# Kernel optimization log

Hardware: AMD Instinct MI355X
Metric: run time of the kernel (lower is better)

The kernel has to match this reference:

```python
import jax, jax.numpy as jnp
import numpy as np
from jax import lax

MEANING_SZ = 512
ARTIC = 64
EMBED = 256
H1 = 512
H2 = 512
SLEN = 32


def _lstm(xs, h0, c0, Wih, Whh, bih, bhh):
    """Single-layer LSTM, torch gate order (i, f, g, o). xs: [S, B, I]."""
    def step(carry, x):
        h, c = carry
        gates = x @ Wih.T + h @ Whh.T + bih + bhh  # [B, 4H]
        i, f, g, o = jnp.split(gates, 4, axis=-1)
        c = jax.nn.sigmoid(f) * c + jax.nn.sigmoid(i) * jnp.tanh(g)
        h = jax.nn.sigmoid(o) * jnp.tanh(c)
        return (h, c), h
    (h, c), ys = lax.scan(step, (h0, c0), xs)
    return ys, (h, c)


def setup_inputs() -> dict:
    key = jax.random.key(0)
    ks = jax.random.split(key, 16)
    s = 0.05
    inp = {
        "ms": jnp.arange(MEANING_SZ, dtype=jnp.int64 if jax.config.jax_enable_x64 else jnp.int32),
        "batches": 16,
        "embedding": jax.random.normal(ks[0], (MEANING_SZ, EMBED), jnp.float32) * s,
        "enc_Wih": jax.random.normal(ks[1], (4 * H1, EMBED), jnp.float32) * s,
        "enc_Whh": jax.random.normal(ks[2], (4 * H1, H1), jnp.float32) * s,
        "enc_bih": jnp.zeros((4 * H1,), jnp.float32),
        "enc_bhh": jnp.zeros((4 * H1,), jnp.float32),
        "enc_init": jax.random.normal(ks[3], (2, H1), jnp.float32) * s,
        "dec_Wih": jax.random.normal(ks[4], (4 * H2, ARTIC), jnp.float32) * s,
        "dec_Whh": jax.random.normal(ks[5], (4 * H2, H2), jnp.float32) * s,
        "dec_bih": jnp.zeros((4 * H2,), jnp.float32),
        "dec_bhh": jnp.zeros((4 * H2,), jnp.float32),
        "dec_init": jax.random.normal(ks[6], (2, H2), jnp.float32) * s,
        "W_param": jax.random.normal(ks[7], (H1, 2 * ARTIC), jnp.float32) * s,
        "W_out": jax.random.normal(ks[8], (H2, MEANING_SZ), jnp.float32) * s,
    }
    return inp


def reference(ms, batches, embedding, enc_Wih, enc_Whh, enc_bih, enc_bhh, enc_init,
              dec_Wih, dec_Whh, dec_bih, dec_bhh, dec_init, W_param, W_out):
    M = embedding.shape[0]
    # --- encoder ---
    embed = embedding[ms]                                   # [M, E]
    xs = jnp.broadcast_to(embed, (SLEN,) + embed.shape)     # same embed repeated S times
    h0 = jnp.broadcast_to(enc_init[0], (M, H1))
    c0 = jnp.broadcast_to(enc_init[1], (M, H1))
    ys, _ = _lstm(xs, h0, c0, enc_Wih, enc_Whh, enc_bih, enc_bhh)  # [S, M, H1]
    params = jax.nn.softplus(jnp.einsum('smh,hp->smp', ys, W_param))  # [S, M, 2A]
    alpha = params[..., 0::2]                               # [S, M, A]
    beta = params[..., 1::2]                                # [S, M, A]
    # --- vectorized Beta reparameterized sampling (replaces triple python loop) ---
    key = jax.random.key(42)
    samp = jax.random.beta(key, alpha, beta, shape=(batches,) + alpha.shape)  # [B, S, M, A]
    # torch.cat along dim=-2 with batch-major blocks -> [S, B*M, A]
    signals = samp.transpose(1, 0, 2, 3).reshape(SLEN, batches * M, ARTIC)
    # --- decoder ---
    hB = jnp.broadcast_to(dec_init[0], (batches * M, H2))
    cB = jnp.broadcast_to(dec_init[1], (batches * M, H2))
    _, (h_last, _) = _lstm(signals, hB, cB, dec_Wih, dec_Whh, dec_bih, dec_bhh)
    logits = h_last @ W_out                                 # [B*M, M]
    return jax.nn.softmax(logits, axis=-1)
```

## Files before the change

### kernel.cpp

```cpp
#include <hip/hip_runtime.h>
#include <cstdint>
#include <cstddef>


namespace {

constexpr int MZ = 512;
constexpr int EMB = 256;
constexpr int H = 512;
constexpr int SL = 32;
constexpr int BT = 16;
constexpr int AR = 64;
constexpr int GG = 4 * H;
constexpr int RD = BT * MZ;
constexpr int SAMP_BLOCKS = 128;
constexpr int MFMA_BLOCKS = (H / 32) * (RD / 128);
constexpr int LROW = 40;

typedef float f32x4 __attribute__((ext_vector_type(4)));
typedef __bf16 bf16x8 __attribute__((ext_vector_type(8)));

struct KK { unsigned a, b; };

__host__ __device__ constexpr unsigned rotl32(unsigned v, int r) {
  return (v << r) | (v >> (32 - r));
}

__host__ __device__ constexpr KK tf(unsigned k0, unsigned k1, unsigned x0, unsigned x1) {
  unsigned k2 = k0 ^ k1 ^ 0x1BD11BDAu;
  x0 += k0; x1 += k1;
  x0 += x1; x1 = rotl32(x1,13); x1 ^= x0;
  x0 += x1; x1 = rotl32(x1,15); x1 ^= x0;
  x0 += x1; x1 = rotl32(x1,26); x1 ^= x0;
  x0 += x1; x1 = rotl32(x1, 6); x1 ^= x0;
  x0 += k1; x1 += k2 + 1u;
  x0 += x1; x1 = rotl32(x1,17); x1 ^= x0;
  x0 += x1; x1 = rotl32(x1,29); x1 ^= x0;
  x0 += x1; x1 = rotl32(x1,16); x1 ^= x0;
  x0 += x1; x1 = rotl32(x1,24); x1 ^= x0;
  x0 += k2; x1 += k0 + 2u;
  x0 += x1; x1 = rotl32(x1,13); x1 ^= x0;
  x0 += x1; x1 = rotl32(x1,15); x1 ^= x0;
  x0 += x1; x1 = rotl32(x1,26); x1 ^= x0;
  x0 += x1; x1 = rotl32(x1, 6); x1 ^= x0;
  x0 += k0; x1 += k1 + 3u;
  x0 += x1; x1 = rotl32(x1,17); x1 ^= x0;
  x0 += x1; x1 = rotl32(x1,29); x1 ^= x0;
  x0 += x1; x1 = rotl32(x1,16); x1 ^= x0;
  x0 += x1; x1 = rotl32(x1,24); x1 ^= x0;
  x0 += k1; x1 += k2 + 4u;
  x0 += x1; x1 = rotl32(x1,13); x1 ^= x0;
  x0 += x1; x1 = rotl32(x1,15); x1 ^= x0;
  x0 += x1; x1 = rotl32(x1,26); x1 ^= x0;
  x0 += x1; x1 = rotl32(x1, 6); x1 ^= x0;
  x0 += k2; x1 += k0 + 5u;
  return KK{x0, x1};
}

constexpr KK KEYA = tf(0u, 42u, 0u, 0u);
constexpr KK KEYB = tf(0u, 42u, 0u, 1u);

__device__ __forceinline__ void split2(KK k, KK& o0, KK& o1) {
  o0 = tf(k.a, k.b, 0u, 0u); o1 = tf(k.a, k.b, 0u, 1u);
}

__device__ __forceinline__ void split3(KK k, KK& o0, KK& o1, KK& o2) {
  o0 = tf(k.a, k.b, 0u, 0u); o1 = tf(k.a, k.b, 0u, 1u); o2 = tf(k.a, k.b, 0u, 2u);
}

__device__ __forceinline__ KK elem_key(KK gk, unsigned j) {
  return tf(gk.a, gk.b, 0u, j);
}

__device__ __forceinline__ unsigned rb32(KK k) {
  KK r = tf(k.a, k.b, 0u, 0u);
  return r.a ^ r.b;
}

__device__ __forceinline__ float u01_from_bits(unsigned bits) {
  return __uint_as_float(0x3F800000u | (bits >> 9)) - 1.0f;
}
__device__ __forceinline__ float uniform01(KK k) {
  return u01_from_bits(rb32(k));
}

__device__ float erfinv_xla(float x) {
  float xx = __fmul_rn(x, x);
  float w = -log1pf(-xx);
  float p;
  if (w < 5.0f) {
    w = __fsub_rn(w, 2.5f);
    p = 2.81022636e-08f;
    p = __fadd_rn(3.43273939e-07f, __fmul_rn(p, w));
    p = __fadd_rn(-3.5233877e-06f, __fmul_rn(p, w));
    p = __fadd_rn(-4.39150654e-06f, __fmul_rn(p, w));
    p = __fadd_rn(0.00021858087f, __fmul_rn(p, w));
    p = __fadd_rn(-0.00125372503f, __fmul_rn(p, w));
    p = __fadd_rn(-0.00417768164f, __fmul_rn(p, w));
    p = __fadd_rn(0.246640727f, __fmul_rn(p, w));
    p = __fadd_rn(1.50140941f, __fmul_rn(p, w));
  } else {
    w = __fsub_rn(__fsqrt_rn(w), 3.0f);
    p = -0.000200214257f;
    p = __fadd_rn(0.000100950558f, __fmul_rn(p, w));
    p = __fadd_rn(0.00134934322f, __fmul_rn(p, w));
    p = __fadd_rn(-0.00367342844f, __fmul_rn(p, w));
    p = __fadd_rn(0.00573950773f, __fmul_rn(p, w));
    p = __fadd_rn(-0.0076224613f, __fmul_rn(p, w));
    p = __fadd_rn(0.00943887047f, __fmul_rn(p, w));
    p = __fadd_rn(1.00167406f, __fmul_rn(p, w));
    p = __fadd_rn(2.83297682f, __fmul_rn(p, w));
  }
  return __fmul_rn(p, x);
}

__device__ __forceinline__ float normal_f(KK k) {
  float f = u01_from_bits(rb32(k));
  const float lo = __uint_as_float(0xBF7FFFFFu);
  float u = __fadd_rn(__fmul_rn(f, 2.0f), lo);
  u = fmaxf(lo, u);
  return __fmul_rn(__uint_as_float(0x3FB504F3u), erfinv_xla(u));
}

__device__ float loggamma_one(KK ekey, float alpha_orig) {
  KK key, sub;
  split2(ekey, key, sub);
  float u_boost = uniform01(sub);
  const bool boost = (alpha_orig >= 1.0f);
  const float al = boost ? alpha_orig : __fadd_rn(alpha_orig, 1.0f);
  const float third = (float)(1.0 / 3.0);
  const float d = __fsub_rn(al, third);
  const float c = __fdiv_rn(third, __fsqrt_rn(d));
  float X, V;
  for (;;) {
    KK nk, xk, uk;
    split3(key, nk, xk, uk);
    key = nk;
    float x, v;
    KK kk = xk;
    do {
      KK k2, ns;
      split2(kk, k2, ns);
      kk = k2;
      x = normal_f(ns);
      v = __fadd_rn(1.0f, __fmul_rn(x, c));
    } while (v <= 0.0f);
    X = __fmul_rn(x, x);
    V = __fmul_rn(__fmul_rn(v, v), v);
    float U = uniform01(uk);
    float sq = __fsub_rn(1.0f, __fmul_rn(0.0331f, __fmul_rn(X, X)));
    if (U < sq) break;
    float rhs = __fadd_rn(__fmul_rn(0.5f, X),
                          __fmul_rn(d, __fadd_rn(__fsub_rn(1.0f, V), logf(V))));
    if (logf(U) < rhs) break;
  }
  float ls = __fadd_rn(logf(d), logf(V));
  if (!boost)
    ls = __fadd_rn(ls, __fdiv_rn(log1pf(-u_boost), alpha_orig));
  return ls;
}

__device__ __forceinline__ float sigm(float x) { return 1.0f / (1.0f + expf(-x)); }

__device__ __forceinline__ unsigned short f2bf(float x) {
  unsigned u = __float_as_uint(x);
  unsigned r = (u + 0x7fffu + ((u >> 16) & 1u)) >> 16;
  return (unsigned short)r;
}
__device__ __forceinline__ float bf2f(unsigned short h) {
  return __uint_as_float(((unsigned)h) << 16);
}
__device__ __forceinline__ void split_bf(float x, unsigned short& hi, unsigned short& lo) {
  hi = f2bf(x);
  lo = f2bf(x - bf2f(hi));
}

__device__ __forceinline__ void beta_sample(const float* __restrict__ alphaA,
                                            const float* __restrict__ betaA,
                                            unsigned short* __restrict__ sigHi,
                                            unsigned short* __restrict__ sigLo,
                                            unsigned idx, int s) {
  unsigned r = idx >> 6;
  unsigned j = idx & 63u;
  unsigned b = r >> 9;
  unsigned m = r & 511u;
  size_t ab = ((size_t)s * MZ + m) * AR + j;
  float alpha = alphaA[ab];
  float beta = betaA[ab];
  unsigned jl = ((b * 32u + (unsigned)s) * 512u + m) * 64u + j;
  float lga = loggamma_one(elem_key(KEYA, jl), alpha);
  float lgb = loggamma_one(elem_key(KEYB, jl), beta);
  float lm = fmaxf(lga, lgb);
  float ea = expf(__fsub_rn(lga, lm));
  float eb = expf(__fsub_rn(lgb, lm));
  float sv = __fdiv_rn(ea, __fadd_rn(ea, eb));
  split_bf(sv, sigHi[idx], sigLo[idx]);
}

}


__global__ __launch_bounds__(256) void fill_sentinel_r17(float* o, int n) {
  int i = blockIdx.x * 256 + threadIdx.x;
  if (i < n) o[i] = 12345.0f;
}

__global__ __launch_bounds__(256) void init_states_r17(const float* __restrict__ encI,
                                                       const float* __restrict__ decI,
                                                       float* __restrict__ hE, float* __restrict__ cE,
                                                       float* __restrict__ hD, float* __restrict__ cD) {
  int idx = blockIdx.x * 256 + threadIdx.x;
  int u = idx & (H - 1);
  if (idx < MZ * H) { hE[idx] = encI[u]; cE[idx] = encI[H + u]; }
  hD[idx] = decI[u]; cD[idx] = decI[H + u];
}

__global__ __launch_bounds__(256) void prep_dec_r17(const float* __restrict__ Wih,
                                                    const float* __restrict__ Whh,
                                                    const float* __restrict__ b1,
                                                    const float* __restrict__ b2,
                                                    unsigned short* __restrict__ WihHi,
                                                    unsigned short* __restrict__ WihLo,
                                                    unsigned short* __restrict__ WhhHi,
                                                    unsigned short* __restrict__ WhhLo,
                                                    float* __restrict__ bsum,
                                                    const float* __restrict__ hD,
                                                    unsigned short* __restrict__ hHi,
                                                    unsigned short* __restrict__ hLo) {
  int idx = blockIdx.x * 256 + threadIdx.x;
  split_bf(Whh[idx], WhhHi[idx], WhhLo[idx]);
  if (idx < GG * AR) split_bf(Wih[idx], WihHi[idx], WihLo[idx]);
  if (idx < GG) bsum[idx] = b1[idx] + b2[idx];
  for (int i = idx; i < RD * H; i += GG * H) split_bf(hD[i], hHi[i], hLo[i]);
}

template <int MODE>
__global__ __launch_bounds__(256) void gemm_abt_r17(const float* __restrict__ A,
                                                    const float* __restrict__ B,
                                                    float* __restrict__ C,
                                                    const float* __restrict__ X1,
                                                    const float* __restrict__ X2,
                                                    int M, int N, int K) {
  __shared__ float As[16][68];
  __shared__ float Bs[16][68];
  int tid = threadIdx.x;
  int tx = tid & 15, ty = tid >> 4;
  int n0 = blockIdx.x * 64, m0 = blockIdx.y * 64;
  int lr = tid >> 2, lk4 = (tid & 3) * 4;
  float acc[4][4] = {};
  for (int k0 = 0; k0 < K; k0 += 16) {
    float4 a4 = *reinterpret_cast<const float4*>(A + (size_t)(m0 + lr) * K + k0 + lk4);
    float4 b4 = *reinterpret_cast<const float4*>(B + (size_t)(n0 + lr) * K + k0 + lk4);
    __syncthreads();
    As[lk4 + 0][lr] = a4.x; As[lk4 + 1][lr] = a4.y; As[lk4 + 2][lr] = a4.z; As[lk4 + 3][lr] = a4.w;
    Bs[lk4 + 0][lr] = b4.x; Bs[lk4 + 1][lr] = b4.y; Bs[lk4 + 2][lr] = b4.z; Bs[lk4 + 3][lr] = b4.w;
    __syncthreads();
#pragma unroll
    for (int k = 0; k < 16; ++k) {
      float av[4], bv[4];
#pragma unroll
      for (int i = 0; i < 4; ++i) av[i] = As[k][ty * 4 + i];
#pragma unroll
      for (int j = 0; j < 4; ++j) bv[j] = Bs[k][tx * 4 + j];
#pragma unroll
      for (int i = 0; i < 4; ++i)
#pragma unroll
        for (int j = 0; j < 4; ++j) acc[i][j] = fmaf(av[i], bv[j], acc[i][j]);
    }
  }
#pragma unroll
  for (int i = 0; i < 4; ++i) {
    int m = m0 + ty * 4 + i;
#pragma unroll
    for (int j = 0; j < 4; ++j) {
      int n = n0 + tx * 4 + j;
      float v = acc[i][j];
      if (MODE == 1) v += X1[n] + X2[n];
      if (MODE == 2) v += X1[(size_t)m * N + n];
      C[(size_t)m * N + n] = v;
    }
  }
}

__global__ __launch_bounds__(256) void mfma_step_r17(
    const unsigned short* __restrict__ sigHi, const unsigned short* __restrict__ sigLo,
    const unsigned short* __restrict__ hHiIn, const unsigned short* __restrict__ hLoIn,
    const unsigned short* __restrict__ WihHi, const unsigned short* __restrict__ WihLo,
    const unsigned short* __restrict__ WhhHi, const unsigned short* __restrict__ WhhLo,
    const float* __restrict__ bsum,
    float* __restrict__ hD, float* __restrict__ cD,
    unsigned short* __restrict__ hHiOut, unsigned short* __restrict__ hLoOut,
    int writeHF,
    const float* __restrict__ alphaA, const float* __restrict__ betaA,
    unsigned short* __restrict__ sigHiNext, unsigned short* __restrict__ sigLoNext,
    int sNext, int nSamp) {
  __shared__ __align__(16) unsigned short AhiS[128 * LROW];
  __shared__ __align__(16) unsigned short AloS[128 * LROW];
  __shared__ __align__(16) unsigned short BhiS[128 * LROW];
  __shared__ __align__(16) unsigned short BloS[128 * LROW];
  int bid = blockIdx.x;
  if (bid < nSamp) {
    unsigned base = bid * 256 + threadIdx.x;
    unsigned stride = (unsigned)nSamp * 256;
    for (unsigned idx = base; idx < (unsigned)(RD * AR); idx += stride)
      beta_sample(alphaA, betaA, sigHiNext, sigLoNext, idx, sNext);
    return;
  }
  bid -= nSamp;
  int ub = bid & 15;
  int mb = bid >> 4;
  int mbBase = mb * 128;
  int ubBase = ub * 32;
  int tid = threadIdx.x;
  int lane = tid & 63, wid = tid >> 6;
  int wr = wid >> 1, wu = wid & 1;
  int lr = lane & 15;
  int lk = (lane >> 4) * 8;
  int srow = tid >> 2;
  int scol = (tid & 3) * 8;
  f32x4 acc[4][4] = {};
  for (int ks = 0; ks < 18; ++ks) {
    int k0 = ks * 32;
    const unsigned short* Ah; const unsigned short* Al;
    const unsigned short* Bh; const unsigned short* Bl;
    int K, kk;
    if (k0 < 64) { Ah = sigHi; Al = sigLo; Bh = WihHi; Bl = WihLo; K = AR; kk = k0; }
    else         { Ah = hHiIn; Al = hLoIn; Bh = WhhHi; Bl = WhhLo; K = H;  kk = k0 - 64; }
    __syncthreads();
#pragma unroll
    for (int q = 0; q < 2; ++q) {
      int row = q * 64 + srow;
      size_t asrc = (size_t)(mbBase + row) * K + kk + scol;
      int g = row >> 5, uu = row & 31;
      size_t bsrc = (size_t)(g * 512 + ubBase + uu) * K + kk + scol;
      int ldst = row * LROW + scol;
      *reinterpret_cast<bf16x8*>(&AhiS[ldst]) = *reinterpret_cast<const bf16x8*>(Ah + asrc);
      *reinterpret_cast<bf16x8*>(&AloS[ldst]) = *reinterpret_cast<const bf16x8*>(Al + asrc);
      *reinterpret_cast<bf16x8*>(&BhiS[ldst]) = *reinterpret_cast<const bf16x8*>(Bh + bsrc);
      *reinterpret_cast<bf16x8*>(&BloS[ldst]) = *reinterpret_cast<const bf16x8*>(Bl + bsrc);
    }
    __syncthreads();
    bf16x8 ah[4], al[4], bh[4], bl[4];
#pragma unroll
    for (int f = 0; f < 4; ++f) {
      int arow = wr * 64 + f * 16 + lr;
      ah[f] = *reinterpret_cast<const bf16x8*>(&AhiS[arow * LROW + lk]);
      al[f] = *reinterpret_cast<const bf16x8*>(&AloS[arow * LROW + lk]);
      int brow = f * 32 + wu * 16 + lr;
      bh[f] = *reinterpret_cast<const bf16x8*>(&BhiS[brow * LROW + lk]);
      bl[f] = *reinterpret_cast<const bf16x8*>(&BloS[brow * LROW + lk]);
    }
#pragma unroll
    for (int i = 0; i < 4; ++i)
#pragma unroll
      for (int g = 0; g < 4; ++g) {
        acc[i][g] = __builtin_amdgcn_mfma_f32_16x16x32_bf16(ah[i], bh[g], acc[i][g], 0, 0, 0);
        acc[i][g] = __builtin_amdgcn_mfma_f32_16x16x32_bf16(ah[i], bl[g], acc[i][g], 0, 0, 0);
        acc[i][g] = __builtin_amdgcn_mfma_f32_16x16x32_bf16(al[i], bh[g], acc[i][g], 0, 0, 0);
      }
  }
  int m0 = mbBase + wr * 64;
  int crow = (lane >> 4) * 4;
  int u = ubBase + wu * 16 + (lane & 15);
  float bi = bsum[u], bff = bsum[u + 512], bg = bsum[u + 1024], bo = bsum[u + 1536];
#pragma unroll
  for (int i = 0; i < 4; ++i) {
#pragma unroll
    for (int r = 0; r < 4; ++r) {
      int m = m0 + i * 16 + crow + r;
      size_t idx = (size_t)m * H + u;
      float gi = acc[i][0][r] + bi;
      float gf = acc[i][1][r] + bff;
      float gg = acc[i][2][r] + bg;
      float go = acc[i][3][r] + bo;
      float cn = sigm(gf) * cD[idx] + sigm(gi) * tanhf(gg);
      float hn = sigm(go) * tanhf(cn);
      cD[idx] = cn;
      if (writeHF) hD[idx] = hn;
      split_bf(hn, hHiOut[idx], hLoOut[idx]);
    }
  }
}

template <int EPI>
__global__ __launch_bounds__(256) void gemm_ab_r17(const float* __restrict__ A,
                                                   const float* __restrict__ B,
                                                   float* __restrict__ C0,
                                                   float* __restrict__ C1,
                                                   int M, int N, int K) {
  __shared__ float As[16][68];
  __shared__ float Bs[16][68];
  int tid = threadIdx.x;
  int tx = tid & 15, ty = tid >> 4;
  int n0 = blockIdx.x * 64, m0 = blockIdx.y * 64;
  int lr = tid >> 2, lk4 = (tid & 3) * 4;
  int bk = tid >> 4, bn4 = (tid & 15) * 4;
  float acc[4][4] = {};
  for (int k0 = 0; k0 < K; k0 += 16) {
    float4 a4 = *reinterpret_cast<const float4*>(A + (size_t)(m0 + lr) * K + k0 + lk4);
    float4 b4 = *reinterpret_cast<const float4*>(B + (size_t)(k0 + bk) * N + n0 + bn4);
    __syncthreads();
    As[lk4 + 0][lr] = a4.x; As[lk4 + 1][lr] = a4.y; As[lk4 + 2][lr] = a4.z; As[lk4 + 3][lr] = a4.w;
    *reinterpret_cast<float4*>(&Bs[bk][bn4]) = b4;
    __syncthreads();
#pragma unroll
    for (int k = 0; k < 16; ++k) {
      float av[4], bv[4];
#pragma unroll
      for (int i = 0; i < 4; ++i) av[i] = As[k][ty * 4 + i];
#pragma unroll
      for (int j = 0; j < 4; ++j) bv[j] = Bs[k][tx * 4 + j];
#pragma unroll
      for (int i = 0; i < 4; ++i)
#pragma unroll
        for (int j = 0; j < 4; ++j) acc[i][j] = fmaf(av[i], bv[j], acc[i][j]);
    }
  }
#pragma unroll
  for (int i = 0; i < 4; ++i) {
    size_t m = (size_t)(m0 + ty * 4 + i);
#pragma unroll
    for (int j = 0; j < 4; ++j) {
      int n = n0 + tx * 4 + j;
      float v = acc[i][j];
      if (EPI == 0) {
        C0[m * N + n] = v;
      } else {
        float sp = fmaxf(v, 0.0f) + log1pf(expf(-fabsf(v)));
        if (n & 1) C1[m * (N / 2) + (n >> 1)] = sp;
        else       C0[m * (N / 2) + (n >> 1)] = sp;
      }
    }
  }
}

__global__ __launch_bounds__(256) void lstm_update_r17(float* __restrict__ h, float* __restrict__ c,
                                                       const float* __restrict__ gates,
                                                       float* __restrict__ ysOut) {
  int idx = blockIdx.x * 256 + threadIdx.x;
  int r = idx >> 9, u = idx & (H - 1);
  const float* g = gates + (size_t)r * GG;
  float gi = g[u], gf = g[u + H], gg = g[u + 2 * H], go = g[u + 3 * H];
  float cn = sigm(gf) * c[idx] + sigm(gi) * tanhf(gg);
  float hn = sigm(go) * tanhf(cn);
  c[idx] = cn; h[idx] = hn;
  if (ysOut) ysOut[idx] = hn;
}

__global__ __launch_bounds__(256) void sample_beta_r17(const float* __restrict__ alphaA,
                                                       const float* __restrict__ betaA,
                                                       unsigned short* __restrict__ sigHi,
                                                       unsigned short* __restrict__ sigLo,
                                                       int s) {
  unsigned idx = blockIdx.x * 256 + threadIdx.x;
  beta_sample(alphaA, betaA, sigHi, sigLo, idx, s);
}

__global__ __launch_bounds__(256) void softmax_rows_r17(const float* __restrict__ L,
                                                        float* __restrict__ O) {
  __shared__ float red[8];
  int r = blockIdx.x;
  const float* row = L + (size_t)r * H;
  int t = threadIdx.x;
  float a = row[t], b = row[t + 256];
  float m = fmaxf(a, b);
#pragma unroll
  for (int o = 1; o < 64; o <<= 1) m = fmaxf(m, __shfl_xor(m, o));
  if ((t & 63) == 0) red[t >> 6] = m;
  __syncthreads();
  m = fmaxf(fmaxf(red[0], red[1]), fmaxf(red[2], red[3]));
  float e0 = expf(a - m), e1 = expf(b - m);
  float s = e0 + e1;
#pragma unroll
  for (int o = 1; o < 64; o <<= 1) s += __shfl_xor(s, o);
  if ((t & 63) == 0) red[4 + (t >> 6)] = s;
  __syncthreads();
  s = red[4] + red[5] + red[6] + red[7];
  O[(size_t)r * H + t] = e0 / s;
  O[(size_t)r * H + t + 256] = e1 / s;
}


extern "C" void kernel_launch(void* const* d_in, const int* in_sizes, int n_in,
                              void* d_out, int out_size, void* d_ws, size_t ws_size,
                              hipStream_t stream) {
  (void)in_sizes; (void)n_in;
  const float* embedding = (const float*)d_in[2];
  const float* eWih = (const float*)d_in[3];
  const float* eWhh = (const float*)d_in[4];
  const float* ebih = (const float*)d_in[5];
  const float* ebhh = (const float*)d_in[6];
  const float* eInit = (const float*)d_in[7];
  const float* dWih = (const float*)d_in[8];
  const float* dWhh = (const float*)d_in[9];
  const float* dbih = (const float*)d_in[10];
  const float* dbhh = (const float*)d_in[11];
  const float* dInit = (const float*)d_in[12];
  const float* Wp = (const float*)d_in[13];
  const float* Wo = (const float*)d_in[14];
  float* out = (float*)d_out;
  float* w = (float*)d_ws;

  size_t o = 0;
  float* xW     = w + o; o += (size_t)MZ * GG;
  float* hE     = w + o; o += (size_t)MZ * H;
  float* cE     = w + o; o += (size_t)MZ * H;
  float* ys     = w + o; o += (size_t)SL * MZ * H;
  float* alphaA = w + o; o += (size_t)SL * MZ * AR;
  float* betaA  = w + o; o += (size_t)SL * MZ * AR;
  float* hD     = w + o; o += (size_t)RD * H;
  float* cD     = w + o; o += (size_t)RD * H;
  float* regB   = w + o; o += (size_t)RD * GG / 4;
  float* logits = w + o; o += (size_t)RD * H;
  float* sig1F  = w + o; o += (size_t)RD * AR;
  if (ws_size < o * sizeof(float)) {
    fill_sentinel_r17<<<(out_size + 255) / 256, 256, 0, stream>>>(out, out_size);
    return;
  }

  unsigned short* sig0Hi = (unsigned short*)ys;
  unsigned short* sig0Lo = sig0Hi + (size_t)RD * AR;
  unsigned short* h0Hi  = sig0Lo + (size_t)RD * AR;
  unsigned short* h0Lo  = h0Hi + (size_t)RD * H;
  unsigned short* WihHi = h0Lo + (size_t)RD * H;
  unsigned short* WihLo = WihHi + (size_t)GG * AR;
  unsigned short* WhhHi = WihLo + (size_t)GG * AR;
  unsigned short* WhhLo = WhhHi + (size_t)GG * H;
  float* bsum = (float*)(WhhLo + (size_t)GG * H);
  unsigned short* h1Hi = (unsigned short*)regB;
  unsigned short* h1Lo = h1Hi + (size_t)RD * H;
  unsigned short* sig1Hi = (unsigned short*)sig1F;
  unsigned short* sig1Lo = sig1Hi + (size_t)RD * AR;

  init_states_r17<<<(RD * H) / 256, 256, 0, stream>>>(eInit, dInit, hE, cE, hD, cD);

  float* egates = logits;
  gemm_abt_r17<1><<<dim3(GG / 64, MZ / 64), 256, 0, stream>>>(embedding, eWih, xW, ebih, ebhh, MZ, GG, EMB);
  for (int s = 0; s < SL; ++s) {
    gemm_abt_r17<2><<<dim3(GG / 64, MZ / 64), 256, 0, stream>>>(hE, eWhh, egates, xW, nullptr, MZ, GG, H);
    lstm_update_r17<<<(MZ * H) / 256, 256, 0, stream>>>(hE, cE, egates, ys + (size_t)s * MZ * H);
  }

  gemm_ab_r17<1><<<dim3(128 / 64, (SL * MZ) / 64), 256, 0, stream>>>(ys, Wp, alphaA, betaA, SL * MZ, 128, H);

  prep_dec_r17<<<(GG * H) / 256, 256, 0, stream>>>(dWih, dWhh, dbih, dbhh,
                                                   WihHi, WihLo, WhhHi, WhhLo, bsum,
                                                   hD, h0Hi, h0Lo);

  sample_beta_r17<<<(RD * AR) / 256, 256, 0, stream>>>(alphaA, betaA, sig0Hi, sig0Lo, 0);

  for (int s = 0; s < SL; ++s) {
    const unsigned short* sHi = (s & 1) ? sig1Hi : sig0Hi;
    const unsigned short* sLo = (s & 1) ? sig1Lo : sig0Lo;
    unsigned short* snHi = (s & 1) ? sig0Hi : sig1Hi;
    unsigned short* snLo = (s & 1) ? sig0Lo : sig1Lo;
    const unsigned short* hiIn = (s & 1) ? h1Hi : h0Hi;
    const unsigned short* loIn = (s & 1) ? h1Lo : h0Lo;
    unsigned short* hiOut = (s & 1) ? h0Hi : h1Hi;
    unsigned short* loOut = (s & 1) ? h0Lo : h1Lo;
    int nSamp = (s < SL - 1) ? SAMP_BLOCKS : 0;
    mfma_step_r17<<<nSamp + MFMA_BLOCKS, 256, 0, stream>>>(
        sHi, sLo, hiIn, loIn, WihHi, WihLo, WhhHi, WhhLo, bsum,
        hD, cD, hiOut, loOut, (s == SL - 1) ? 1 : 0,
        alphaA, betaA, snHi, snLo, s + 1, nSamp);
  }

  gemm_ab_r17<0><<<dim3(H / 64, RD / 64), 256, 0, stream>>>(hD, Wo, logits, nullptr, RD, H, H);
  softmax_rows_r17<<<RD, 256, 0, stream>>>(logits, out);
}
```

Measured before the change: 5.080 ms.

## Run decoder LSTM as persistent cooperative kernel with grid sync and register cell state

Replaces the 32 per-step decoder kernel launches with one cooperative persistent kernel of 1024 blocks that loops over time steps and separates them with grid.sync. The cell state now stays in registers instead of going to global memory, and every block samples its share of the next step's Beta noise. Block-to-tile mapping is arranged by XCD, and the LDS row pitch shrinks from 40 to 36. The risks are grid-sync cost, occupancy limits for cooperative launch (it falls back to the old path on failure), and possible LDS bank conflicts with the new pitch.

```diff
diff --git a/kernel.cpp b/kernel.cpp
--- a/kernel.cpp
+++ b/kernel.cpp
@@ -1,7 +1,10 @@
 #include <hip/hip_runtime.h>
+#include <hip/hip_cooperative_groups.h>
 #include <cstdint>
 #include <cstddef>
 
+
+namespace cg = cooperative_groups;
 
 namespace {
 
@@ -13,9 +16,9 @@
 constexpr int AR = 64;
 constexpr int GG = 4 * H;
 constexpr int RD = BT * MZ;
+constexpr int LROW = 36;
 constexpr int SAMP_BLOCKS = 128;
 constexpr int MFMA_BLOCKS = (H / 32) * (RD / 128);
-constexpr int LROW = 40;
 
 typedef float f32x4 __attribute__((ext_vector_type(4)));
 typedef __bf16 bf16x8 __attribute__((ext_vector_type(8)));
@@ -197,15 +200,19 @@
   split_bf(sv, sigHi[idx], sigLo[idx]);
 }
 
-}
-
-
-__global__ __launch_bounds__(256) void fill_sentinel_r17(float* o, int n) {
+struct StepPtrs {
+  const unsigned short *sHi, *sLo, *hInHi, *hInLo;
+};
+
+}
+
+
+__global__ __launch_bounds__(256) void fill_sentinel_r19(float* o, int n) {
   int i = blockIdx.x * 256 + threadIdx.x;
   if (i < n) o[i] = 12345.0f;
 }
 
-__global__ __launch_bounds__(256) void init_states_r17(const float* __restrict__ encI,
+__global__ __launch_bounds__(256) void init_states_r19(const float* __restrict__ encI,
                                                        const float* __restrict__ decI,
                                                        float* __restrict__ hE, float* __restrict__ cE,
                                                        float* __restrict__ hD, float* __restrict__ cD) {
@@ -215,7 +222,7 @@
   hD[idx] = decI[u]; cD[idx] = decI[H + u];
 }
 
-__global__ __launch_bounds__(256) void prep_dec_r17(const float* __restrict__ Wih,
+__global__ __launch_bounds__(256) void prep_dec_r19(const float* __restrict__ Wih,
                                                     const float* __restrict__ Whh,
                                                     const float* __restrict__ b1,
                                                     const float* __restrict__ b2,
@@ -235,7 +242,7 @@
 }
 
 template <int MODE>
-__global__ __launch_bounds__(256) void gemm_abt_r17(const float* __restrict__ A,
+__global__ __launch_bounds__(256) void gemm_abt_r19(const float* __restrict__ A,
                                                     const float* __restrict__ B,
                                                     float* __restrict__ C,
                                                     const float* __restrict__ X1,
@@ -282,7 +289,125 @@
   }
 }
 
-__global__ __launch_bounds__(256) void mfma_step_r17(
+__global__ __launch_bounds__(256, 4) void dec_persist_r19(
+    unsigned short* sig0Hi, unsigned short* sig0Lo,
+    unsigned short* sig1Hi, unsigned short* sig1Lo,
+    unsigned short* h0Hi, unsigned short* h0Lo,
+    unsigned short* h1Hi, unsigned short* h1Lo,
+    const unsigned short* __restrict__ WihHi, const unsigned short* __restrict__ WihLo,
+    const unsigned short* __restrict__ WhhHi, const unsigned short* __restrict__ WhhLo,
+    const float* __restrict__ bsum, float* __restrict__ hD,
+    const float* __restrict__ cInit,
+    const float* __restrict__ alphaA, const float* __restrict__ betaA) {
+  __shared__ __align__(16) unsigned short AhiS[128 * LROW];
+  __shared__ __align__(16) unsigned short AloS[128 * LROW];
+  __shared__ __align__(16) unsigned short BhiS[128 * LROW];
+  __shared__ __align__(16) unsigned short BloS[128 * LROW];
+  cg::grid_group grid = cg::this_grid();
+  int bid = blockIdx.x;
+  int xcd = bid & 7, idxx = bid >> 3;
+  int mb = xcd * 8 + (idxx >> 4);
+  int ub = idxx & 15;
+  int mbBase = mb * 128;
+  int ubBase = ub * 32;
+  int tid = threadIdx.x;
+  int lane = tid & 63, wid = tid >> 6;
+  int wr = wid >> 1, wu = wid & 1;
+  int lr = lane & 15;
+  int lk = (lane >> 4) * 8;
+  int srow = tid >> 2;
+  int scol = (tid & 3) * 8;
+  int m0 = mbBase + wr * 64;
+  int crow = (lane >> 4) * 4;
+  int u = ubBase + wu * 16 + (lane & 15);
+  float bi = bsum[u], bff = bsum[u + 512], bg = bsum[u + 1024], bo = bsum[u + 1536];
+  float creg[4][4];
+  {
+    float c0 = cInit[u];
+#pragma unroll
+    for (int i = 0; i < 4; ++i)
+#pragma unroll
+      for (int r = 0; r < 4; ++r) creg[i][r] = c0;
+  }
+  for (int s = 0; s < SL; ++s) {
+    const unsigned short *sHi, *sLo, *hInHi, *hInLo;
+    unsigned short *hOutHi, *hOutLo, *snHi, *snLo;
+    if (s & 1) {
+      sHi = sig1Hi; sLo = sig1Lo; hInHi = h1Hi; hInLo = h1Lo;
+      hOutHi = h0Hi; hOutLo = h0Lo; snHi = sig0Hi; snLo = sig0Lo;
+    } else {
+      sHi = sig0Hi; sLo = sig0Lo; hInHi = h0Hi; hInLo = h0Lo;
+      hOutHi = h1Hi; hOutLo = h1Lo; snHi = sig1Hi; snLo = sig1Lo;
+    }
+    if (s < SL - 1) {
+      unsigned base = (unsigned)bid * 256 + tid;
+      beta_sample(alphaA, betaA, snHi, snLo, base, s + 1);
+      beta_sample(alphaA, betaA, snHi, snLo, base + 262144u, s + 1);
+    }
+    f32x4 acc[4][4] = {};
+    for (int ks = 0; ks < 18; ++ks) {
+      int k0 = ks * 32;
+      const unsigned short* Ah; const unsigned short* Al;
+      const unsigned short* Bh; const unsigned short* Bl;
+      int K, kk;
+      if (k0 < 64) { Ah = sHi; Al = sLo; Bh = WihHi; Bl = WihLo; K = AR; kk = k0; }
+      else         { Ah = hInHi; Al = hInLo; Bh = WhhHi; Bl = WhhLo; K = H; kk = k0 - 64; }
+      __syncthreads();
+#pragma unroll
+      for (int q = 0; q < 2; ++q) {
+        int row = q * 64 + srow;
+        size_t asrc = (size_t)(mbBase + row) * K + kk + scol;
+        int g = row >> 5, uu = row & 31;
+        size_t bsrc = (size_t)(g * 512 + ubBase + uu) * K + kk + scol;
+        int ldst = row * LROW + scol;
+        *reinterpret_cast<bf16x8*>(&AhiS[ldst]) = *reinterpret_cast<const bf16x8*>(Ah + asrc);
+        *reinterpret_cast<bf16x8*>(&AloS[ldst]) = *reinterpret_cast<const bf16x8*>(Al + asrc);
+        *reinterpret_cast<bf16x8*>(&BhiS[ldst]) = *reinterpret_cast<const bf16x8*>(Bh + bsrc);
+        *reinterpret_cast<bf16x8*>(&BloS[ldst]) = *reinterpret_cast<const bf16x8*>(Bl + bsrc);
+      }
+      __syncthreads();
+      bf16x8 ah[4], al[4], bh[4], bl[4];
+#pragma unroll
+      for (int f = 0; f < 4; ++f) {
+        int arow = wr * 64 + f * 16 + lr;
+        ah[f] = *reinterpret_cast<const bf16x8*>(&AhiS[arow * LROW + lk]);
+        al[f] = *reinterpret_cast<const bf16x8*>(&AloS[arow * LROW + lk]);
+        int brow = f * 32 + wu * 16 + lr;
+        bh[f] = *reinterpret_cast<const bf16x8*>(&BhiS[brow * LROW + lk]);
+        bl[f] = *reinterpret_cast<const bf16x8*>(&BloS[brow * LROW + lk]);
+      }
+#pragma unroll
+      for (int i = 0; i < 4; ++i)
+#pragma unroll
+        for (int g = 0; g < 4; ++g) {
+          acc[i][g] = __builtin_amdgcn_mfma_f32_16x16x32_bf16(ah[i], bh[g], acc[i][g], 0, 0, 0);
+          acc[i][g] = __builtin_amdgcn_mfma_f32_16x16x32_bf16(ah[i], bl[g], acc[i][g], 0, 0, 0);
+          acc[i][g] = __builtin_amdgcn_mfma_f32_16x16x32_bf16(al[i], bh[g], acc[i][g], 0, 0, 0);
+        }
+    }
+#pragma unroll
+    for (int i = 0; i < 4; ++i) {
+#pragma unroll
+      for (int r = 0; r < 4; ++r) {
+        int m = m0 + i * 16 + crow + r;
+        size_t idx = (size_t)m * H + u;
+        float gi = acc[i][0][r] + bi;
+        float gf = acc[i][1][r] + bff;
+        float gg = acc[i][2][r] + bg;
+        float go = acc[i][3][r] + bo;
+        float cn = sigm(gf) * creg[i][r] + sigm(gi) * tanhf(gg);
+        float hn = sigm(go) * tanhf(cn);
+        creg[i][r] = cn;
+        if (s == SL - 1) hD[idx] = hn;
+        split_bf(hn, hOutHi[idx], hOutLo[idx]);
+      }
+    }
+    __threadfence();
+    grid.sync();
+  }
+}
+
+__global__ __launch_bounds__(256) void mfma_step_r19(
     const unsigned short* __restrict__ sigHi, const unsigned short* __restrict__ sigLo,
     const unsigned short* __restrict__ hHiIn, const unsigned short* __restrict__ hLoIn,
     const unsigned short* __restrict__ WihHi, const unsigned short* __restrict__ WihLo,
@@ -383,7 +508,7 @@
 }
 
 template <int EPI>
-__global__ __launch_bounds__(256) void gemm_ab_r17(const float* __restrict__ A,
+__global__ __launch_bounds__(256) void gemm_ab_r19(const float* __restrict__ A,
                                                    const float* __restrict__ B,
                                                    float* __restrict__ C0,
                                                    float* __restrict__ C1,
@@ -434,7 +559,7 @@
   }
 }
 
-__global__ __launch_bounds__(256) void lstm_update_r17(float* __restrict__ h, float* __restrict__ c,
+__global__ __launch_bounds__(256) void lstm_update_r19(float* __restrict__ h, float* __restrict__ c,
                                                        const float* __restrict__ gates,
                                                        float* __restrict__ ysOut) {
   int idx = blockIdx.x * 256 + threadIdx.x;
@@ -447,7 +572,7 @@
   if (ysOut) ysOut[idx] = hn;
 }
 
-__global__ __launch_bounds__(256) void sample_beta_r17(const float* __restrict__ alphaA,
+__global__ __launch_bounds__(256) void sample_beta_r19(const float* __restrict__ alphaA,
                                                        const float* __restrict__ betaA,
                                                        unsigned short* __restrict__ sigHi,
                                                        unsigned short* __restrict__ sigLo,
@@ -456,7 +581,7 @@
   beta_sample(alphaA, betaA, sigHi, sigLo, idx, s);
 }
 
-__global__ __launch_bounds__(256) void softmax_rows_r17(const float* __restrict__ L,
+__global__ __launch_bounds__(256) void softmax_rows_r19(const float* __restrict__ L,
                                                         float* __restrict__ O) {
   __shared__ float red[8];
   int r = blockIdx.x;
@@ -514,7 +639,7 @@
   float* logits = w + o; o += (size_t)RD * H;
   float* sig1F  = w + o; o += (size_t)RD * AR;
   if (ws_size < o * sizeof(float)) {
-    fill_sentinel_r17<<<(out_size + 255) / 256, 256, 0, stream>>>(out, out_size);
+    fill_sentinel_r19<<<(out_size + 255) / 256, 256, 0, stream>>>(out, out_size);
     return;
   }
 
@@ -532,39 +657,51 @@
   unsigned short* sig1Hi = (unsigned short*)sig1F;
   unsigned short* sig1Lo = sig1Hi + (size_t)RD * AR;
 
-  init_states_r17<<<(RD * H) / 256, 256, 0, stream>>>(eInit, dInit, hE, cE, hD, cD);
+  init_states_r19<<<(RD * H) / 256, 256, 0, stream>>>(eInit, dInit, hE, cE, hD, cD);
 
   float* egates = logits;
-  gemm_abt_r17<1><<<dim3(GG / 64, MZ / 64), 256, 0, stream>>>(embedding, eWih, xW, ebih, ebhh, MZ, GG, EMB);
+  gemm_abt_r19<1><<<dim3(GG / 64, MZ / 64), 256, 0, stream>>>(embedding, eWih, xW, ebih, ebhh, MZ, GG, EMB);
   for (int s = 0; s < SL; ++s) {
-    gemm_abt_r17<2><<<dim3(GG / 64, MZ / 64), 256, 0, stream>>>(hE, eWhh, egates, xW, nullptr, MZ, GG, H);
-    lstm_update_r17<<<(MZ * H) / 256, 256, 0, stream>>>(hE, cE, egates, ys + (size_t)s * MZ * H);
-  }
-
-  gemm_ab_r17<1><<<dim3(128 / 64, (SL * MZ) / 64), 256, 0, stream>>>(ys, Wp, alphaA, betaA, SL * MZ, 128, H);
-
-  prep_dec_r17<<<(GG * H) / 256, 256, 0, stream>>>(dWih, dWhh, dbih, dbhh,
+    gemm_abt_r19<2><<<dim3(GG / 64, MZ / 64), 256, 0, stream>>>(hE, eWhh, egates, xW, nullptr, MZ, GG, H);
+    lstm_update_r19<<<(MZ * H) / 256, 256, 0, stream>>>(hE, cE, egates, ys + (size_t)s * MZ * H);
+  }
+
+  gemm_ab_r19<1><<<dim3(128 / 64, (SL * MZ) / 64), 256, 0, stream>>>(ys, Wp, alphaA, betaA, SL * MZ, 128, H);
+
+  prep_dec_r19<<<(GG * H) / 256, 256, 0, stream>>>(dWih, dWhh, dbih, dbhh,
                                                    WihHi, WihLo, WhhHi, WhhLo, bsum,
                                                    hD, h0Hi, h0Lo);
 
-  sample_beta_r17<<<(RD * AR) / 256, 256, 0, stream>>>(alphaA, betaA, sig0Hi, sig0Lo, 0);
-
-  for (int s = 0; s < SL; ++s) {
-    const unsigned short* sHi = (s & 1) ? sig1Hi : sig0Hi;
-    const unsigned short* sLo = (s & 1) ? sig1Lo : sig0Lo;
-    unsigned short* snHi = (s & 1) ? sig0Hi : sig1Hi;
-    unsigned short* snLo = (s & 1) ? sig0Lo : sig1Lo;
-    const unsigned short* hiIn = (s & 1) ? h1Hi : h0Hi;
-    const unsigned short* loIn = (s & 1) ? h1Lo : h0Lo;
-    unsigned short* hiOut = (s & 1) ? h0Hi : h1Hi;
-    unsigned short* loOut = (s & 1) ? h0Lo : h1Lo;
-    int nSamp = (s < SL - 1) ? SAMP_BLOCKS : 0;
-    mfma_step_r17<<<nSamp + MFMA_BLOCKS, 256, 0, stream>>>(
-        sHi, sLo, hiIn, loIn, WihHi, WihLo, WhhHi, WhhLo, bsum,
-        hD, cD, hiOut, loOut, (s == SL - 1) ? 1 : 0,
-        alphaA, betaA, snHi, snLo, s + 1, nSamp);
-  }
-
-  gemm_ab_r17<0><<<dim3(H / 64, RD / 64), 256, 0, stream>>>(hD, Wo, logits, nullptr, RD, H, H);
-  softmax_rows_r17<<<RD, 256, 0, stream>>>(logits, out);
-}
+  sample_beta_r19<<<(RD * AR) / 256, 256, 0, stream>>>(alphaA, betaA, sig0Hi, sig0Lo, 0);
+
+  const float* cInit = dInit + H;
+  void* args[] = {
+    (void*)&sig0Hi, (void*)&sig0Lo, (void*)&sig1Hi, (void*)&sig1Lo,
+    (void*)&h0Hi, (void*)&h0Lo, (void*)&h1Hi, (void*)&h1Lo,
+    (void*)&WihHi, (void*)&WihLo, (void*)&WhhHi, (void*)&WhhLo,
+    (void*)&bsum, (void*)&hD, (void*)&cInit,
+    (void*)&alphaA, (void*)&betaA
+  };
+  hipError_t cerr = hipLaunchCooperativeKernel((const void*)dec_persist_r19,
+                                               dim3(1024), dim3(256), args, 0, stream);
+  if (cerr != hipSuccess) {
+    for (int s = 0; s < SL; ++s) {
+      const unsigned short* sHi = (s & 1) ? sig1Hi : sig0Hi;
+      const unsigned short* sLo = (s & 1) ? sig1Lo : sig0Lo;
+      unsigned short* snHi = (s & 1) ? sig0Hi : sig1Hi;
+      unsigned short* snLo = (s & 1) ? sig0Lo : sig1Lo;
+      const unsigned short* hiIn = (s & 1) ? h1Hi : h0Hi;
+      const unsigned short* loIn = (s & 1) ? h1Lo : h0Lo;
+      unsigned short* hiOut = (s & 1) ? h0Hi : h1Hi;
+      unsigned short* loOut = (s & 1) ? h0Lo : h1Lo;
+      int nSamp = (s < SL - 1) ? SAMP_BLOCKS : 0;
+      mfma_step_r19<<<nSamp + MFMA_BLOCKS, 256, 0, stream>>>(
+          sHi, sLo, hiIn, loIn, WihHi, WihLo, WhhHi, WhhLo, bsum,
+          hD, cD, hiOut, loOut, (s == SL - 1) ? 1 : 0,
+          alphaA, betaA, snHi, snLo, s + 1, nSamp);
+    }
+  }
+
+  gemm_ab_r19<0><<<dim3(H / 64, RD / 64), 256, 0, stream>>>(hD, Wo, logits, nullptr, RD, H, H);
+  softmax_rows_r19<<<RD, 256, 0, stream>>>(logits, out);
+}
```

Result: slower. 14.28 ms (+181.1%).
